# Kernel optimization log

Hardware: AMD Instinct MI355X
Metric: run time of the kernel (lower is better)

Reference implementation:

```python
import jax, jax.numpy as jnp
import numpy as np

B, T, S, H, A = 512, 2048, 16, 128, 4
EPS = 1e-8


def setup_inputs() -> dict:
    key = jax.random.key(0)
    ks = jax.random.split(key, 8)
    sc = lambda fan_in: 1.0 / np.sqrt(fan_in)
    return {
        "state": jax.random.normal(ks[0], (B, T, S), dtype=jnp.float32),
        "Wc1": jax.random.normal(ks[1], (S, H), dtype=jnp.float32) * sc(S),
        "bc1": jnp.zeros((H,), jnp.float32),
        "Wc2": jax.random.normal(ks[2], (H, A), dtype=jnp.float32) * sc(H),
        "bc2": jnp.zeros((A,), jnp.float32),
        "Wh1": jax.random.normal(ks[3], (S, H), dtype=jnp.float32) * sc(S),
        "bh1": jnp.zeros((H,), jnp.float32),
        "wh2": jax.random.normal(ks[4], (H,), dtype=jnp.float32) * sc(H),
        "bh2": jnp.zeros((1,), jnp.float32),
        "Wf": jax.random.normal(ks[5], (S, S), dtype=jnp.float32) * sc(S),
        "bf": jnp.zeros((S,), jnp.float32),
        "Wg": jax.random.normal(ks[6], (S, S * A), dtype=jnp.float32) * sc(S),
        "bg": jnp.zeros((S * A,), jnp.float32),
    }


def reference(state, Wc1, bc1, Wc2, bc2, Wh1, bh1, wh2, bh2, Wf, bf, Wg, bg):
    # reference controller: 2-layer MLP -> u_ref = -2 * controller(state)  [B,T,A]
    u_ref = -2.0 * (jnp.tanh(state @ Wc1 + bc1) @ Wc2 + bc2)

    # CBF h(state): MLP -> scalar per (B,T)
    def cbf(s):
        return jnp.tanh(s @ Wh1 + bh1) @ wh2 + bh2[0]  # [B,T]

    h = cbf(state)
    # delta_h = d h / d state  [B,T,S]  (torch autograd.grad on summed h)
    delta_h = jax.grad(lambda s: cbf(s).sum())(state)

    # control-affine dynamics: f [B,T,S], g [B,T,S,A]
    f = state @ Wf + bf
    g = (state @ Wg + bg).reshape(B, T, S, A)

    # CBF-QP constraint:  left . u <= right
    left = -jnp.einsum('bts,btsa->bta', delta_h, g)          # [B,T,A]
    right = h + jnp.einsum('bts,bts->bt', delta_h, f)        # [B,T]

    # QP: min 1/2 u^T I u + u_ref^T u  s.t. left.u <= right
    # Closed-form KKT solution (single inequality, identity Hessian):
    u_unc = -u_ref                                            # [B,T,A]
    viol = jnp.einsum('bta,bta->bt', left, u_unc) - right     # [B,T]
    lam = jax.nn.relu(viol) / (jnp.sum(left * left, axis=-1) + EPS)
    u = u_unc - lam[..., None] * left                         # [B,T,A]
    return u
```

## Files before the change

### kernel.cpp

```cpp
#include <hip/hip_runtime.h>
#include <hip/hip_bf16.h>

#define HDIM 128
#define SDIM 16
#define ADIM 4
#define NTOK (512 * 2048)
#define NTILE (NTOK / 16)
#define NBLK 2048
#define WPB 4
#define TPW (NTILE / (NBLK * WPB))

typedef _Float16 half4 __attribute__((ext_vector_type(4)));
typedef float f32x4 __attribute__((ext_vector_type(4)));

__device__ __forceinline__ f32x4 mm(half4 a, half4 b, f32x4 c) {
    return __builtin_amdgcn_mfma_f32_16x16x16f16(a, b, c, 0, 0, 0);
}
__device__ __forceinline__ float fast_tanh(float x) {
    float e = __expf(2.0f * x);
    return 1.0f - 2.0f * __builtin_amdgcn_rcpf(e + 1.0f);
}
__device__ __forceinline__ f32x4 tanh4(f32x4 z) {
    f32x4 r;
    r.x = fast_tanh(z.x); r.y = fast_tanh(z.y);
    r.z = fast_tanh(z.z); r.w = fast_tanh(z.w);
    return r;
}
__device__ __forceinline__ half4 toh(f32x4 v) {
    half4 h;
    h.x = (_Float16)v.x; h.y = (_Float16)v.y;
    h.z = (_Float16)v.z; h.w = (_Float16)v.w;
    return h;
}
__device__ __forceinline__ void split4(f32x4 v, half4& hi, half4& lo) {
    hi = toh(v);
    f32x4 r;
    r.x = v.x - (float)hi.x; r.y = v.y - (float)hi.y;
    r.z = v.z - (float)hi.z; r.w = v.w - (float)hi.w;
    lo = toh(r);
}
__device__ __forceinline__ float dot4(f32x4 a, f32x4 b) {
    return a.x*b.x + a.y*b.y + a.z*b.z + a.w*b.w;
}
__device__ __forceinline__ float redq(float v) {
    v += __shfl_xor(v, 16, 64);
    v += __shfl_xor(v, 32, 64);
    return v;
}

__global__ __launch_bounds__(256, 4) void cbf_qp_kernel(
    const float* __restrict__ state,
    const float* __restrict__ Wc1, const float* __restrict__ bc1,
    const float* __restrict__ Wc2, const float* __restrict__ bc2,
    const float* __restrict__ Wh1, const float* __restrict__ bh1,
    const float* __restrict__ wh2, const float* __restrict__ bh2,
    const float* __restrict__ Wf,  const float* __restrict__ bf,
    const float* __restrict__ Wg,  const float* __restrict__ bg,
    float* __restrict__ out)
{
    __shared__ __align__(16) half4 az1_s[8 * 64];
    __shared__ __align__(16) half4 aua_s[8 * 64];
    __shared__ __align__(16) half4 az2h_s[8 * 64];
    __shared__ __align__(16) half4 az2l_s[8 * 64];
    __shared__ __align__(16) half4 adhh_s[8 * 64];
    __shared__ __align__(16) half4 adhl_s[8 * 64];
    __shared__ __align__(16) half4 afh_s[64];
    __shared__ __align__(16) half4 afl_s[64];
    __shared__ __align__(16) half4 agh_s[4 * 64];
    __shared__ __align__(16) half4 agl_s[4 * 64];
    __shared__ __align__(16) float bgt_s[64];
    __shared__ __align__(16) float bc1_s[HDIM];
    __shared__ __align__(16) float bh1_s[HDIM];
    __shared__ __align__(16) float wh2_s[HDIM];

    const int tid = threadIdx.x;

    for (int idx = tid; idx < 8 * 64; idx += 256) {
        const int c = idx >> 6, lane = idx & 63;
        const int m = lane & 15, q = lane >> 4;
        half4 hz1, hua, h2h, h2l, hdh, hdl;
        #pragma unroll
        for (int e = 0; e < 4; ++e) {
            const int k = q * 4 + e;
            const int j = c * 16 + k;
            hz1[e] = (_Float16)Wc1[k * HDIM + c*16 + m];
            hua[e] = (m < ADIM) ? (_Float16)Wc2[j * ADIM + m] : (_Float16)0.f;
            float w2 = Wh1[k * HDIM + c*16 + m];
            _Float16 hh = (_Float16)w2;
            h2h[e] = hh; h2l[e] = (_Float16)(w2 - (float)hh);
            float wd = Wh1[m * HDIM + j] * wh2[j];
            _Float16 hd = (_Float16)wd;
            hdh[e] = hd; hdl[e] = (_Float16)(wd - (float)hd);
        }
        az1_s[idx] = hz1;  aua_s[idx] = hua;
        az2h_s[idx] = h2h; az2l_s[idx] = h2l;
        adhh_s[idx] = hdh; adhl_s[idx] = hdl;
    }
    if (tid < 64) {
        const int m = tid & 15, q = tid >> 4;
        half4 fh, fl;
        #pragma unroll
        for (int e = 0; e < 4; ++e) {
            float w = Wf[(q*4+e) * SDIM + m];
            _Float16 h = (_Float16)w;
            fh[e] = h; fl[e] = (_Float16)(w - (float)h);
        }
        afh_s[tid] = fh; afl_s[tid] = fl;
    }
    {
        const int a = tid >> 6, lane = tid & 63;
        const int m = lane & 15, q = lane >> 4;
        half4 gh, gl;
        #pragma unroll
        for (int e = 0; e < 4; ++e) {
            float w = Wg[(q*4+e) * 64 + m*4 + a];
            _Float16 h = (_Float16)w;
            gh[e] = h; gl[e] = (_Float16)(w - (float)h);
        }
        agh_s[tid] = gh; agl_s[tid] = gl;
    }
    if (tid < 64)
        bgt_s[(tid >> 4) * 16 + (tid & 15)] = bg[(tid & 15) * 4 + (tid >> 4)];
    if (tid < HDIM) {
        bc1_s[tid] = bc1[tid];
        bh1_s[tid] = bh1[tid];
        wh2_s[tid] = wh2[tid];
    }
    __syncthreads();

    const int lane = tid & 63;
    const int q = lane >> 4, n = lane & 15;
    const int wid = blockIdx.x * WPB + (tid >> 6);

    f32x4 bfC = *(const f32x4*)(bf + q*4);
    f32x4 uaC;
    {
        f32x4 b2 = *(const f32x4*)(bc2);
        uaC.x = q == 0 ? b2.x : 0.f; uaC.y = q == 0 ? b2.y : 0.f;
        uaC.z = q == 0 ? b2.z : 0.f; uaC.w = q == 0 ? b2.w : 0.f;
    }
    f32x4 bgC0 = *(const f32x4*)(&bgt_s[0*16 + q*4]);
    f32x4 bgC1 = *(const f32x4*)(&bgt_s[1*16 + q*4]);
    f32x4 bgC2 = *(const f32x4*)(&bgt_s[2*16 + q*4]);
    f32x4 bgC3 = *(const f32x4*)(&bgt_s[3*16 + q*4]);
    const float bh2v = bh2[0];

    for (int it = 0; it < TPW; ++it) {
        const int tile = wid * TPW + it;
        f32x4 sv = *(const f32x4*)(state + (size_t)(tile*16 + n) * SDIM + q*4);
        half4 bsh, bsl;
        split4(sv, bsh, bsl);

        f32x4 uaA = uaC, uaB = {0.f, 0.f, 0.f, 0.f};
        f32x4 dhA = {0.f, 0.f, 0.f, 0.f};
        f32x4 dhB = {0.f, 0.f, 0.f, 0.f};
        f32x4 dhC = {0.f, 0.f, 0.f, 0.f};
        float hp0 = 0.f, hp1 = 0.f;
        #pragma unroll 2
        for (int c = 0; c < 8; ++c) {
            f32x4 b1 = *(const f32x4*)(&bc1_s[c*16 + q*4]);
            f32x4 z1 = mm(az1_s[c*64 + lane], bsh, b1);
            half4 t1h = toh(tanh4(z1));
            if (c & 1) uaB = mm(aua_s[c*64 + lane], t1h, uaB);
            else       uaA = mm(aua_s[c*64 + lane], t1h, uaA);

            f32x4 b2v = *(const f32x4*)(&bh1_s[c*16 + q*4]);
            half4 a2h = az2h_s[c*64 + lane];
            f32x4 z2 = mm(a2h, bsl, b2v);
            z2 = mm(az2l_s[c*64 + lane], bsh, z2);
            z2 = mm(a2h, bsh, z2);
            f32x4 t2 = tanh4(z2);
            f32x4 s2;
            s2.x = 1.f - t2.x*t2.x; s2.y = 1.f - t2.y*t2.y;
            s2.z = 1.f - t2.z*t2.z; s2.w = 1.f - t2.w*t2.w;
            half4 s2h, s2l;
            split4(s2, s2h, s2l);
            half4 adh_h = adhh_s[c*64 + lane];
            dhA = mm(adh_h, s2h, dhA);
            dhB = mm(adhl_s[c*64 + lane], s2h, dhB);
            dhC = mm(adh_h, s2l, dhC);

            f32x4 wv = *(const f32x4*)(&wh2_s[c*16 + q*4]);
            if (c & 1) hp1 += dot4(wv, t2);
            else       hp0 += dot4(wv, t2);
        }
        f32x4 ua = uaA + uaB;
        f32x4 dh = dhA + dhB + dhC;
        float hp = hp0 + hp1;

        half4 fh = afh_s[lane], fl = afl_s[lane];
        f32x4 fD = mm(fh, bsl, bfC);
        fD = mm(fl, bsh, fD);
        fD = mm(fh, bsh, fD);
        f32x4 G0, G1, G2, G3;
        {
            half4 gh = agh_s[0*64 + lane], gl = agl_s[0*64 + lane];
            G0 = mm(gh, bsl, bgC0); G0 = mm(gl, bsh, G0); G0 = mm(gh, bsh, G0);
        }
        {
            half4 gh = agh_s[1*64 + lane], gl = agl_s[1*64 + lane];
            G1 = mm(gh, bsl, bgC1); G1 = mm(gl, bsh, G1); G1 = mm(gh, bsh, G1);
        }
        {
            half4 gh = agh_s[2*64 + lane], gl = agl_s[2*64 + lane];
            G2 = mm(gh, bsl, bgC2); G2 = mm(gl, bsh, G2); G2 = mm(gh, bsh, G2);
        }
        {
            half4 gh = agh_s[3*64 + lane], gl = agl_s[3*64 + lane];
            G3 = mm(gh, bsl, bgC3); G3 = mm(gl, bsh, G3); G3 = mm(gh, bsh, G3);
        }

        float right = redq(hp + dot4(dh, fD)) + bh2v;
        float l0 = -redq(dot4(dh, G0));
        float l1 = -redq(dot4(dh, G1));
        float l2 = -redq(dot4(dh, G2));
        float l3 = -redq(dot4(dh, G3));
        float u0 = 2.f * redq(ua.x);
        float u1 = 2.f * redq(ua.y);
        float u2 = 2.f * redq(ua.z);
        float u3 = 2.f * redq(ua.w);

        float viol = l0*u0 + l1*u1 + l2*u2 + l3*u3 - right;
        float lsq  = l0*l0 + l1*l1 + l2*l2 + l3*l3;
        float lam  = viol > 0.f ? viol / (lsq + 1e-8f) : 0.f;

        if (q == 0) {
            f32x4 uo;
            uo.x = u0 - lam*l0; uo.y = u1 - lam*l1;
            uo.z = u2 - lam*l2; uo.w = u3 - lam*l3;
            *(f32x4*)(out + (size_t)(tile*16 + n) * ADIM) = uo;
        }
    }
}

extern "C" void kernel_launch(void* const* d_in, const int* in_sizes, int n_in,
                              void* d_out, int out_size, void* d_ws, size_t ws_size,
                              hipStream_t stream) {
    (void)in_sizes; (void)n_in; (void)d_ws; (void)ws_size; (void)out_size;
    const float* state = (const float*)d_in[0];
    const float* Wc1   = (const float*)d_in[1];
    const float* bc1   = (const float*)d_in[2];
    const float* Wc2   = (const float*)d_in[3];
    const float* bc2   = (const float*)d_in[4];
    const float* Wh1   = (const float*)d_in[5];
    const float* bh1   = (const float*)d_in[6];
    const float* wh2   = (const float*)d_in[7];
    const float* bh2   = (const float*)d_in[8];
    const float* Wf    = (const float*)d_in[9];
    const float* bf    = (const float*)d_in[10];
    const float* Wg    = (const float*)d_in[11];
    const float* bg    = (const float*)d_in[12];
    float* out = (float*)d_out;

    hipLaunchKernelGGL(cbf_qp_kernel, dim3(NBLK), dim3(256), 0, stream,
                       state, Wc1, bc1, Wc2, bc2, Wh1, bh1, wh2, bh2,
                       Wf, bf, Wg, bg, out);
}
```

Before: 223.4 us.

## Process two token tiles per iteration with prefetched state loads

Each wave now handles two 16-token tiles per loop iteration and interleaves their independent MFMA chains, which gives the scheduler more instruction-level parallelism. The next pair's state vectors are prefetched from global memory so load latency overlaps compute. tanh now calls exp2 directly with a pre-scaled argument, and bias loads for G move from registers to LDS inside the loop. The cost is higher register pressure, which may reduce occupancy.

Result: no change. 224.7 us (+0.6%).

```diff
diff --git a/kernel.cpp b/kernel.cpp
--- a/kernel.cpp
+++ b/kernel.cpp
@@ -17,7 +17,7 @@
     return __builtin_amdgcn_mfma_f32_16x16x16f16(a, b, c, 0, 0, 0);
 }
 __device__ __forceinline__ float fast_tanh(float x) {
-    float e = __expf(2.0f * x);
+    float e = __builtin_amdgcn_exp2f(x * 2.88539008177792681f);
     return 1.0f - 2.0f * __builtin_amdgcn_rcpf(e + 1.0f);
 }
 __device__ __forceinline__ f32x4 tanh4(f32x4 z) {
@@ -131,6 +131,7 @@
     const int lane = tid & 63;
     const int q = lane >> 4, n = lane & 15;
     const int wid = blockIdx.x * WPB + (tid >> 6);
+    const int base = wid * TPW;
 
     f32x4 bfC = *(const f32x4*)(bf + q*4);
     f32x4 uaC;
@@ -139,97 +140,147 @@
         uaC.x = q == 0 ? b2.x : 0.f; uaC.y = q == 0 ? b2.y : 0.f;
         uaC.z = q == 0 ? b2.z : 0.f; uaC.w = q == 0 ? b2.w : 0.f;
     }
-    f32x4 bgC0 = *(const f32x4*)(&bgt_s[0*16 + q*4]);
-    f32x4 bgC1 = *(const f32x4*)(&bgt_s[1*16 + q*4]);
-    f32x4 bgC2 = *(const f32x4*)(&bgt_s[2*16 + q*4]);
-    f32x4 bgC3 = *(const f32x4*)(&bgt_s[3*16 + q*4]);
     const float bh2v = bh2[0];
 
-    for (int it = 0; it < TPW; ++it) {
-        const int tile = wid * TPW + it;
-        f32x4 sv = *(const f32x4*)(state + (size_t)(tile*16 + n) * SDIM + q*4);
-        half4 bsh, bsl;
-        split4(sv, bsh, bsl);
-
-        f32x4 uaA = uaC, uaB = {0.f, 0.f, 0.f, 0.f};
-        f32x4 dhA = {0.f, 0.f, 0.f, 0.f};
-        f32x4 dhB = {0.f, 0.f, 0.f, 0.f};
-        f32x4 dhC = {0.f, 0.f, 0.f, 0.f};
-        float hp0 = 0.f, hp1 = 0.f;
+    f32x4 sv0 = *(const f32x4*)(state + (size_t)((base + 0)*16 + n) * SDIM + q*4);
+    f32x4 sv1 = *(const f32x4*)(state + (size_t)((base + 1)*16 + n) * SDIM + q*4);
+
+    for (int p = 0; p < TPW/2; ++p) {
+        const int t0 = base + 2*p;
+        const int np = (p + 1 < TPW/2) ? (p + 1) : p;
+        f32x4 nsv0 = *(const f32x4*)(state + (size_t)((base + 2*np    )*16 + n) * SDIM + q*4);
+        f32x4 nsv1 = *(const f32x4*)(state + (size_t)((base + 2*np + 1)*16 + n) * SDIM + q*4);
+
+        half4 bsh0, bsl0, bsh1, bsl1;
+        split4(sv0, bsh0, bsl0);
+        split4(sv1, bsh1, bsl1);
+
+        f32x4 ua0A = uaC, ua0B = {0.f, 0.f, 0.f, 0.f};
+        f32x4 ua1A = uaC, ua1B = {0.f, 0.f, 0.f, 0.f};
+        f32x4 dh0A = {0.f,0.f,0.f,0.f}, dh0B = {0.f,0.f,0.f,0.f}, dh0C = {0.f,0.f,0.f,0.f};
+        f32x4 dh1A = {0.f,0.f,0.f,0.f}, dh1B = {0.f,0.f,0.f,0.f}, dh1C = {0.f,0.f,0.f,0.f};
+        float hp0a = 0.f, hp0b = 0.f, hp1a = 0.f, hp1b = 0.f;
+
         #pragma unroll 2
         for (int c = 0; c < 8; ++c) {
             f32x4 b1 = *(const f32x4*)(&bc1_s[c*16 + q*4]);
-            f32x4 z1 = mm(az1_s[c*64 + lane], bsh, b1);
-            half4 t1h = toh(tanh4(z1));
-            if (c & 1) uaB = mm(aua_s[c*64 + lane], t1h, uaB);
-            else       uaA = mm(aua_s[c*64 + lane], t1h, uaA);
+            half4 a1 = az1_s[c*64 + lane];
+            f32x4 z10 = mm(a1, bsh0, b1);
+            f32x4 z11 = mm(a1, bsh1, b1);
+            half4 t1h0 = toh(tanh4(z10));
+            half4 t1h1 = toh(tanh4(z11));
+            half4 au = aua_s[c*64 + lane];
+            if (c & 1) { ua0B = mm(au, t1h0, ua0B); ua1B = mm(au, t1h1, ua1B); }
+            else       { ua0A = mm(au, t1h0, ua0A); ua1A = mm(au, t1h1, ua1A); }
 
             f32x4 b2v = *(const f32x4*)(&bh1_s[c*16 + q*4]);
             half4 a2h = az2h_s[c*64 + lane];
-            f32x4 z2 = mm(a2h, bsl, b2v);
-            z2 = mm(az2l_s[c*64 + lane], bsh, z2);
-            z2 = mm(a2h, bsh, z2);
-            f32x4 t2 = tanh4(z2);
-            f32x4 s2;
-            s2.x = 1.f - t2.x*t2.x; s2.y = 1.f - t2.y*t2.y;
-            s2.z = 1.f - t2.z*t2.z; s2.w = 1.f - t2.w*t2.w;
-            half4 s2h, s2l;
-            split4(s2, s2h, s2l);
-            half4 adh_h = adhh_s[c*64 + lane];
-            dhA = mm(adh_h, s2h, dhA);
-            dhB = mm(adhl_s[c*64 + lane], s2h, dhB);
-            dhC = mm(adh_h, s2l, dhC);
+            half4 a2l = az2l_s[c*64 + lane];
+            f32x4 z20 = mm(a2h, bsl0, b2v);
+            z20 = mm(a2l, bsh0, z20);
+            z20 = mm(a2h, bsh0, z20);
+            f32x4 z21 = mm(a2h, bsl1, b2v);
+            z21 = mm(a2l, bsh1, z21);
+            z21 = mm(a2h, bsh1, z21);
+            f32x4 t20 = tanh4(z20);
+            f32x4 t21 = tanh4(z21);
+            f32x4 s20, s21;
+            s20.x = 1.f - t20.x*t20.x; s20.y = 1.f - t20.y*t20.y;
+            s20.z = 1.f - t20.z*t20.z; s20.w = 1.f - t20.w*t20.w;
+            s21.x = 1.f - t21.x*t21.x; s21.y = 1.f - t21.y*t21.y;
+            s21.z = 1.f - t21.z*t21.z; s21.w = 1.f - t21.w*t21.w;
+            half4 s2h0, s2l0, s2h1, s2l1;
+            split4(s20, s2h0, s2l0);
+            split4(s21, s2h1, s2l1);
+            half4 adh = adhh_s[c*64 + lane];
+            half4 adl = adhl_s[c*64 + lane];
+            dh0A = mm(adh, s2h0, dh0A);
+            dh0B = mm(adl, s2h0, dh0B);
+            dh0C = mm(adh, s2l0, dh0C);
+            dh1A = mm(adh, s2h1, dh1A);
+            dh1B = mm(adl, s2h1, dh1B);
+            dh1C = mm(adh, s2l1, dh1C);
 
             f32x4 wv = *(const f32x4*)(&wh2_s[c*16 + q*4]);
-            if (c & 1) hp1 += dot4(wv, t2);
-            else       hp0 += dot4(wv, t2);
-        }
-        f32x4 ua = uaA + uaB;
-        f32x4 dh = dhA + dhB + dhC;
-        float hp = hp0 + hp1;
+            if (c & 1) { hp0b += dot4(wv, t20); hp1b += dot4(wv, t21); }
+            else       { hp0a += dot4(wv, t20); hp1a += dot4(wv, t21); }
+        }
+        f32x4 ua0 = ua0A + ua0B;
+        f32x4 ua1 = ua1A + ua1B;
+        f32x4 dh0 = dh0A + dh0B + dh0C;
+        f32x4 dh1 = dh1A + dh1B + dh1C;
+        float hpp0 = hp0a + hp0b;
+        float hpp1 = hp1a + hp1b;
 
         half4 fh = afh_s[lane], fl = afl_s[lane];
-        f32x4 fD = mm(fh, bsl, bfC);
-        fD = mm(fl, bsh, fD);
-        fD = mm(fh, bsh, fD);
-        f32x4 G0, G1, G2, G3;
+        f32x4 fD0 = mm(fh, bsl0, bfC); fD0 = mm(fl, bsh0, fD0); fD0 = mm(fh, bsh0, fD0);
+        f32x4 fD1 = mm(fh, bsl1, bfC); fD1 = mm(fl, bsh1, fD1); fD1 = mm(fh, bsh1, fD1);
+
+        float right0 = redq(hpp0 + dot4(dh0, fD0)) + bh2v;
+        float right1 = redq(hpp1 + dot4(dh1, fD1)) + bh2v;
+
+        float l00, l01, l02, l03, l10, l11, l12, l13;
         {
             half4 gh = agh_s[0*64 + lane], gl = agl_s[0*64 + lane];
-            G0 = mm(gh, bsl, bgC0); G0 = mm(gl, bsh, G0); G0 = mm(gh, bsh, G0);
+            f32x4 bgC = *(const f32x4*)(&bgt_s[0*16 + q*4]);
+            f32x4 Ga = mm(gh, bsl0, bgC); Ga = mm(gl, bsh0, Ga); Ga = mm(gh, bsh0, Ga);
+            f32x4 Gb = mm(gh, bsl1, bgC); Gb = mm(gl, bsh1, Gb); Gb = mm(gh, bsh1, Gb);
+            l00 = -redq(dot4(dh0, Ga));
+            l10 = -redq(dot4(dh1, Gb));
         }
         {
             half4 gh = agh_s[1*64 + lane], gl = agl_s[1*64 + lane];
-            G1 = mm(gh, bsl, bgC1); G1 = mm(gl, bsh, G1); G1 = mm(gh, bsh, G1);
+            f32x4 bgC = *(const f32x4*)(&bgt_s[1*16 + q*4]);
+            f32x4 Ga = mm(gh, bsl0, bgC); Ga = mm(gl, bsh0, Ga); Ga = mm(gh, bsh0, Ga);
+            f32x4 Gb = mm(gh, bsl1, bgC); Gb = mm(gl, bsh1, Gb); Gb = mm(gh, bsh1, Gb);
+            l01 = -redq(dot4(dh0, Ga));
+            l11 = -redq(dot4(dh1, Gb));
         }
         {
             half4 gh = agh_s[2*64 + lane], gl = agl_s[2*64 + lane];
-            G2 = mm(gh, bsl, bgC2); G2 = mm(gl, bsh, G2); G2 = mm(gh, bsh, G2);
+            f32x4 bgC = *(const f32x4*)(&bgt_s[2*16 + q*4]);
+            f32x4 Ga = mm(gh, bsl0, bgC); Ga = mm(gl, bsh0, Ga); Ga = mm(gh, bsh0, Ga);
+            f32x4 Gb = mm(gh, bsl1, bgC); Gb = mm(gl, bsh1, Gb); Gb = mm(gh, bsh1, Gb);
+            l02 = -redq(dot4(dh0, Ga));
+            l12 = -redq(dot4(dh1, Gb));
         }
         {
             half4 gh = agh_s[3*64 + lane], gl = agl_s[3*64 + lane];
-            G3 = mm(gh, bsl, bgC3); G3 = mm(gl, bsh, G3); G3 = mm(gh, bsh, G3);
-        }
-
-        float right = redq(hp + dot4(dh, fD)) + bh2v;
-        float l0 = -redq(dot4(dh, G0));
-        float l1 = -redq(dot4(dh, G1));
-        float l2 = -redq(dot4(dh, G2));
-        float l3 = -redq(dot4(dh, G3));
-        float u0 = 2.f * redq(ua.x);
-        float u1 = 2.f * redq(ua.y);
-        float u2 = 2.f * redq(ua.z);
-        float u3 = 2.f * redq(ua.w);
-
-        float viol = l0*u0 + l1*u1 + l2*u2 + l3*u3 - right;
-        float lsq  = l0*l0 + l1*l1 + l2*l2 + l3*l3;
-        float lam  = viol > 0.f ? viol / (lsq + 1e-8f) : 0.f;
+            f32x4 bgC = *(const f32x4*)(&bgt_s[3*16 + q*4]);
+            f32x4 Ga = mm(gh, bsl0, bgC); Ga = mm(gl, bsh0, Ga); Ga = mm(gh, bsh0, Ga);
+            f32x4 Gb = mm(gh, bsl1, bgC); Gb = mm(gl, bsh1, Gb); Gb = mm(gh, bsh1, Gb);
+            l03 = -redq(dot4(dh0, Ga));
+            l13 = -redq(dot4(dh1, Gb));
+        }
+
+        float u00 = 2.f * redq(ua0.x);
+        float u01 = 2.f * redq(ua0.y);
+        float u02 = 2.f * redq(ua0.z);
+        float u03 = 2.f * redq(ua0.w);
+        float u10 = 2.f * redq(ua1.x);
+        float u11 = 2.f * redq(ua1.y);
+        float u12 = 2.f * redq(ua1.z);
+        float u13 = 2.f * redq(ua1.w);
+
+        float viol0 = l00*u00 + l01*u01 + l02*u02 + l03*u03 - right0;
+        float lsq0  = l00*l00 + l01*l01 + l02*l02 + l03*l03;
+        float lam0  = viol0 > 0.f ? viol0 / (lsq0 + 1e-8f) : 0.f;
+        float viol1 = l10*u10 + l11*u11 + l12*u12 + l13*u13 - right1;
+        float lsq1  = l10*l10 + l11*l11 + l12*l12 + l13*l13;
+        float lam1  = viol1 > 0.f ? viol1 / (lsq1 + 1e-8f) : 0.f;
 
         if (q == 0) {
-            f32x4 uo;
-            uo.x = u0 - lam*l0; uo.y = u1 - lam*l1;
-            uo.z = u2 - lam*l2; uo.w = u3 - lam*l3;
-            *(f32x4*)(out + (size_t)(tile*16 + n) * ADIM) = uo;
-        }
+            f32x4 uo0;
+            uo0.x = u00 - lam0*l00; uo0.y = u01 - lam0*l01;
+            uo0.z = u02 - lam0*l02; uo0.w = u03 - lam0*l03;
+            *(f32x4*)(out + (size_t)(t0*16 + n) * ADIM) = uo0;
+            f32x4 uo1;
+            uo1.x = u10 - lam1*l10; uo1.y = u11 - lam1*l11;
+            uo1.z = u12 - lam1*l12; uo1.w = u13 - lam1*l13;
+            *(f32x4*)(out + (size_t)((t0+1)*16 + n) * ADIM) = uo1;
+        }
+
+        sv0 = nsv0; sv1 = nsv1;
     }
 }
 
```
